# Performance work log

Hardware: AMD Instinct MI355X
Metric: run time of the kernel (lower is better)

## Reference

```python
import jax, jax.numpy as jnp
import numpy as np

# Spec constants (from init_kwargs)
NUM_ANCHORS = 5
NUM_CLASSES = 80
FM_H = 19
FM_W = 19
MAX_OBJECT = 50
NOOBJECT_SCALE = 1.0
OBJECT_SCALE = 5.0
BACKGROUND_THRESHOLD = 0.6
COORD_SCALE = 1.0
CLASS_SCALE = 1.0


def _iou_cwh(a, b):
    """IoU for boxes in (cx, cy, w, h) format; broadcasts over leading dims.
    Matches bbox_iou(..., x1y1x2y2=False) in the torch repo (0 when no overlap)."""
    ax1, ax2 = a[..., 0] - a[..., 2] * 0.5, a[..., 0] + a[..., 2] * 0.5
    ay1, ay2 = a[..., 1] - a[..., 3] * 0.5, a[..., 1] + a[..., 3] * 0.5
    bx1, bx2 = b[..., 0] - b[..., 2] * 0.5, b[..., 0] + b[..., 2] * 0.5
    by1, by2 = b[..., 1] - b[..., 3] * 0.5, b[..., 1] + b[..., 3] * 0.5
    uw = jnp.maximum(ax2, bx2) - jnp.minimum(ax1, bx1)
    uh = jnp.maximum(ay2, by2) - jnp.minimum(ay1, by1)
    cw = a[..., 2] + b[..., 2] - uw
    ch = a[..., 3] + b[..., 3] - uh
    inter = jnp.where((cw > 0) & (ch > 0), cw * ch, 0.0)
    union = a[..., 2] * a[..., 3] + b[..., 2] * b[..., 3] - inter
    return inter / jnp.maximum(union, 1e-12)


def setup_inputs() -> dict:
    key = jax.random.key(0)
    k1, k2, k3, k4, k5 = jax.random.split(key, 5)
    B, A, C, H, W, T = 64, NUM_ANCHORS, NUM_CLASSES, FM_H, FM_W, MAX_OBJECT
    output = jax.random.normal(k1, (B, A * (5 + C), H, W), jnp.float32) * 0.5
    # targets: per object (class, cx, cy, w, h), normalized to [0,1]; list ends at first cx == 0
    cls_t = jax.random.randint(k2, (B, T), 0, C).astype(jnp.float32)
    xy = jax.random.uniform(k3, (B, T, 2), jnp.float32, minval=0.1, maxval=0.9)
    wh = jax.random.uniform(k4, (B, T, 2), jnp.float32, minval=0.05, maxval=0.4)
    nvalid = jax.random.randint(k5, (B,), 1, T + 1)
    valid = (jnp.arange(T)[None, :] < nvalid[:, None]).astype(jnp.float32)
    tgt = jnp.concatenate([cls_t[..., None], xy, wh], axis=-1) * valid[..., None]
    target = tgt.reshape(B, T * 5)
    anchors = jnp.array([[1.3221, 1.73145], [3.19275, 4.00944], [5.05587, 8.09892],
                         [9.47112, 4.84053], [11.2364, 10.0071]], jnp.float32)
    return {"output": output, "target": target, "anchors": anchors}


def reference(output, target, anchors):
    B = output.shape[0]
    A, C, H, W, T = NUM_ANCHORS, NUM_CLASSES, FM_H, FM_W, MAX_OBJECT
    out = output.reshape(B, A, 5 + C, H, W)
    x = jax.nn.sigmoid(out[:, :, 0])
    y = jax.nn.sigmoid(out[:, :, 1])
    w = out[:, :, 2]
    h = out[:, :, 3]
    conf = jax.nn.sigmoid(out[:, :, 4])
    cls_logits = jnp.transpose(out[:, :, 5:], (0, 1, 3, 4, 2))  # [B,A,H,W,C]

    # decoded predicted boxes in grid units (detached for target building, as in torch)
    px = x + jnp.arange(W, dtype=x.dtype)[None, None, None, :]
    py = y + jnp.arange(H, dtype=x.dtype)[None, None, :, None]
    pw = jnp.exp(w) * anchors[None, :, 0, None, None]
    ph = jnp.exp(h) * anchors[None, :, 1, None, None]
    pred = jax.lax.stop_gradient(jnp.stack([px, py, pw, ph], axis=-1))  # [B,A,H,W,4]

    tgt = target.reshape(B, T, 5)
    cls_t = tgt[..., 0]
    gx = tgt[..., 1] * W
    gy = tgt[..., 2] * H
    gw = tgt[..., 3] * W
    gh = tgt[..., 4] * H
    # break-at-first-zero semantics of the torch loop
    valid = jnp.cumprod((tgt[..., 1] != 0).astype(jnp.int32), axis=1).astype(bool)  # [B,T]

    gt_boxes = jnp.stack([gx, gy, gw, gh], axis=-1)  # [B,T,4]
    # all-pairs pred-vs-gt IoU (replaces per-object python loop)
    pred_flat = pred.reshape(B, A * H * W, 4)
    ious = _iou_cwh(pred_flat[:, :, None, :], gt_boxes[:, None, :, :])  # [B,N,T]
    best_iou = jnp.max(jnp.where(valid[:, None, :], ious, 0.0), axis=-1)  # [B,N]
    conf_mask = jnp.where(best_iou > BACKGROUND_THRESHOLD, 0.0, NOOBJECT_SCALE)
    conf_mask = conf_mask.reshape(B, A, H, W)

    # best anchor per gt: IoU of (w,h) boxes centered at origin
    aw = anchors[:, 0][None, None, :]
    ah = anchors[:, 1][None, None, :]
    inter_a = jnp.minimum(gw[..., None], aw) * jnp.minimum(gh[..., None], ah)
    union_a = gw[..., None] * gh[..., None] + aw * ah - inter_a
    best_n = jnp.argmax(inter_a / jnp.maximum(union_a, 1e-12), axis=-1)  # [B,T]

    gi = jnp.clip(gx.astype(jnp.int32), 0, W - 1)
    gj = jnp.clip(gy.astype(jnp.int32), 0, H - 1)
    bidx = jnp.arange(B)[:, None]
    pred_sel = pred[bidx, best_n, gj, gi]  # [B,T,4]
    iou_obj = _iou_cwh(gt_boxes, pred_sel)  # [B,T]

    N = B * A * H * W
    flat = ((bidx * A + best_n) * H + gj) * W + gi  # [B,T]
    flat = jnp.where(valid, flat, N).reshape(-1)  # invalid -> out of range, dropped

    def scat(vals):
        return jnp.zeros((N,), jnp.float32).at[flat].set(
            vals.reshape(-1), mode="drop").reshape(B, A, H, W)

    coord_mask = scat(jnp.ones_like(gx))
    cls_mask = coord_mask
    conf_mask = conf_mask.reshape(-1).at[flat].set(
        jnp.full((B * T,), OBJECT_SCALE, jnp.float32), mode="drop").reshape(B, A, H, W)
    tx = scat(gx - gi.astype(gx.dtype))
    ty = scat(gy - gj.astype(gy.dtype))
    tw = scat(jnp.log(jnp.maximum(gw, 1e-12) / anchors[best_n, 0]))
    th = scat(jnp.log(jnp.maximum(gh, 1e-12) / anchors[best_n, 1]))
    tconf = scat(iou_obj)
    tcls = scat(cls_t)

    # losses (sum reduction, matching MSELoss/CrossEntropyLoss(size_average=False))
    loss_x = COORD_SCALE * jnp.sum((coord_mask * (x - tx)) ** 2) / 2.0
    loss_y = COORD_SCALE * jnp.sum((coord_mask * (y - ty)) ** 2) / 2.0
    loss_w = COORD_SCALE * jnp.sum((coord_mask * (w - tw)) ** 2) / 2.0
    loss_h = COORD_SCALE * jnp.sum((coord_mask * (h - th)) ** 2) / 2.0
    sq = jnp.sqrt(conf_mask)
    loss_conf = jnp.sum((sq * (conf - tconf)) ** 2) / 2.0
    ce = -jnp.take_along_axis(jax.nn.log_softmax(cls_logits, axis=-1),
                              tcls.astype(jnp.int32)[..., None], axis=-1)[..., 0]
    loss_cls = CLASS_SCALE * jnp.sum(cls_mask * ce)
    return loss_x + loss_y + loss_w + loss_h + loss_conf + loss_cls
```

## Files before the change

### kernel.cpp

```cpp
#include <hip/hip_runtime.h>
#include <math.h>

#define NUM_ANCHORS 5
#define NUM_CLASSES 80
#define FM_H 19
#define FM_W 19
#define MAX_OBJECT 50
#define HW (FM_H * FM_W)
#define CELLS_PER_B (NUM_ANCHORS * HW)
#define CH (5 + NUM_CLASSES)
#define THREADS 512
#define NW (THREADS / 64)
#define BLOCKS_PER_B ((CELLS_PER_B + THREADS - 1) / THREADS)
#define OBJECT_SCALE 5.0f
#define BACKGROUND_THRESHOLD 0.6f

__device__ inline float frcp(float v) { return __builtin_amdgcn_rcpf(v); }
__device__ inline float fsigmoid(float v) { return frcp(1.0f + __expf(-v)); }

__global__ __launch_bounds__(THREADS) void yolov2_main(
    const float* __restrict__ out,
    const float* __restrict__ target,
    const float* __restrict__ anchors,
    float* __restrict__ partial)
{
    const int b    = blockIdx.x / BLOCKS_PER_B;
    const int blk  = blockIdx.x % BLOCKS_PER_B;
    const int cell = blk * THREADS + threadIdx.x;
    const int lane = threadIdx.x & 63;
    const int wid  = threadIdx.x >> 6;

    __shared__ float4 gA[MAX_OBJECT];
    __shared__ float4 gB[MAX_OBJECT];
    __shared__ float4 gT[MAX_OBJECT];
    __shared__ int    entries[MAX_OBJECT];
    __shared__ int    nv_sh, ne_sh;
    __shared__ float  wsum[NW];

    const bool incell = (cell < CELLS_PER_B);
    const int a    = incell ? (cell / HW) : 0;
    const int hw   = cell - a * HW;
    const int hrow = hw / FM_W;
    const int wcol = hw - hrow * FM_W;

    const float* base = out + ((size_t)(b * NUM_ANCHORS + a) * CH) * HW + hw;
    float ox = 0.f, oy = 0.f, ow = 0.f, oh = 0.f, oc = 0.f;
    if (incell) {
        ox = base[0];
        oy = base[HW];
        ow = base[2 * HW];
        oh = base[3 * HW];
        oc = base[4 * HW];
    }
    const float anc_w = anchors[2 * a];
    const float anc_h = anchors[2 * a + 1];

    if (threadIdx.x < 64) {
        const int t = threadIdx.x;
        float f0 = 0.f, f1 = 0.f, f2 = 0.f, f3 = 0.f, f4 = 0.f;
        if (t < MAX_OBJECT) {
            const float* tp = target + (size_t)b * MAX_OBJECT * 5 + t * 5;
            f0 = tp[0]; f1 = tp[1]; f2 = tp[2]; f3 = tp[3]; f4 = tp[4];
        }
        unsigned long long m = __ballot(t < MAX_OBJECT && f1 != 0.0f);
        int nv = __popcll(m);
        if (t == 0) nv_sh = nv;

        int acell = 0x7FFFFFFF;
        int icls = 0;
        if (t < MAX_OBJECT) {
            float gx = f1 * (float)FM_W;
            float gy = f2 * (float)FM_H;
            float gw = f3 * (float)FM_W;
            float gh = f4 * (float)FM_H;
            int bn = 0; float best = -1.0f;
            #pragma unroll
            for (int k = 0; k < NUM_ANCHORS; ++k) {
                float aw = anchors[2 * k], ah = anchors[2 * k + 1];
                float inter = fminf(gw, aw) * fminf(gh, ah);
                float uni = gw * gh + aw * ah - inter;
                float r = inter * frcp(fmaxf(uni, 1e-12f));
                if (r > best) { best = r; bn = k; }
            }
            int gi = (int)gx; gi = gi < 0 ? 0 : (gi > FM_W - 1 ? FM_W - 1 : gi);
            int gj = (int)gy; gj = gj < 0 ? 0 : (gj > FM_H - 1 ? FM_H - 1 : gj);
            acell = bn * HW + gj * FM_W + gi;
            icls  = (int)f0;
            gA[t] = make_float4(gx - gw * 0.5f, gx + gw * 0.5f,
                                gy - gh * 0.5f, gy + gh * 0.5f);
            gB[t] = make_float4(gw, gh, gw * gh, __int_as_float(acell));
            gT[t] = make_float4(gx - (float)gi, gy - (float)gj,
                                __logf(fmaxf(gw, 1e-12f) * frcp(anchors[2 * bn])),
                                __logf(fmaxf(gh, 1e-12f) * frcp(anchors[2 * bn + 1])));
        }

        bool owner = (t < nv);
        #pragma unroll
        for (int s = 1; s < MAX_OBJECT; ++s) {
            int other = __shfl(acell, (t + s) & 63, 64);
            owner = owner && !((t + s < nv) && (other == acell));
        }
        bool keep = owner && ((acell >> 9) == blk);
        unsigned long long om = __ballot(keep);
        int pos = __popcll(om & ((1ull << t) - 1ull));
        if (keep) entries[pos] = acell | (icls << 16);
        if (t == 0) ne_sh = __popcll(om);
    }
    __syncthreads();

    const int nv = nv_sh;
    const int ne = ne_sh;
    float local = 0.0f;

    const bool ld = (lane < NUM_CLASSES / 2);
    int  eCur = wid;
    bool hasP = (eCur < ne);
    float pv0 = 0.f, pv1 = 0.f;
    int   pcls = 0;
    if (hasP) {
        int pk = entries[eCur];
        int ec = pk & 0xFFFF;
        pcls   = pk >> 16;
        int ea = ec / HW;
        const float* cl = out + ((size_t)(b * NUM_ANCHORS + ea) * CH + 5) * HW
                              + (ec - ea * HW);
        pv0 = ld ? cl[(2 * lane + 0) * HW] : 0.0f;
        pv1 = ld ? cl[(2 * lane + 1) * HW] : 0.0f;
    }

    if (incell) {
        float x    = fsigmoid(ox);
        float y    = fsigmoid(oy);
        float conf = fsigmoid(oc);
        float px = x + (float)wcol;
        float py = y + (float)hrow;
        float pw = __expf(ow) * anc_w;
        float ph = __expf(oh) * anc_h;
        float ax1 = px - pw * 0.5f, ax2 = px + pw * 0.5f;
        float ay1 = py - ph * 0.5f, ay2 = py + ph * 0.5f;
        float parea = pw * ph;

        bool bg_hit = false;
        int  last_t = -1;
        #pragma unroll 5
        for (int t = 0; t < nv; ++t) {
            float4 A  = gA[t];
            float4 Bv = gB[t];
            float uw = fmaxf(ax2, A.y) - fminf(ax1, A.x);
            float uh = fmaxf(ay2, A.w) - fminf(ay1, A.z);
            float cw  = Bv.x + pw - uw;
            float chh = Bv.y + ph - uh;
            float inter = (cw > 0.f && chh > 0.f) ? cw * chh : 0.f;
            float uni = parea + Bv.z - inter;
            bg_hit = bg_hit || (inter > BACKGROUND_THRESHOLD * uni);
            if (__float_as_int(Bv.w) == cell) last_t = t;
        }

        if (last_t >= 0) {
            float4 A  = gA[last_t];
            float4 Bv = gB[last_t];
            float4 Tt = gT[last_t];
            float uw = fmaxf(ax2, A.y) - fminf(ax1, A.x);
            float uh = fmaxf(ay2, A.w) - fminf(ay1, A.z);
            float cw  = Bv.x + pw - uw;
            float chh = Bv.y + ph - uh;
            float inter = (cw > 0.f && chh > 0.f) ? cw * chh : 0.f;
            float tconf = inter * frcp(fmaxf(parea + Bv.z - inter, 1e-12f));
            float dc = conf - tconf; local += 0.5f * OBJECT_SCALE * dc * dc;
            float dx = x  - Tt.x; local += 0.5f * dx * dx;
            float dy = y  - Tt.y; local += 0.5f * dy * dy;
            float dw = ow - Tt.z; local += 0.5f * dw * dw;
            float dh = oh - Tt.w; local += 0.5f * dh * dh;
        } else if (!bg_hit) {
            local += 0.5f * conf * conf;
        }
    }

    while (hasP) {
        int  eNxt = eCur + NW;
        bool hasN = (eNxt < ne);
        float nv0 = 0.f, nv1 = 0.f;
        int   ncls = 0;
        if (hasN) {
            int pk = entries[eNxt];
            int ec = pk & 0xFFFF;
            ncls   = pk >> 16;
            int ea = ec / HW;
            const float* cl = out + ((size_t)(b * NUM_ANCHORS + ea) * CH + 5) * HW
                                  + (ec - ea * HW);
            nv0 = ld ? cl[(2 * lane + 0) * HW] : 0.0f;
            nv1 = ld ? cl[(2 * lane + 1) * HW] : 0.0f;
        }
        float s = ld ? (__expf(pv0) + __expf(pv1)) : 0.0f;
        #pragma unroll
        for (int off = 32; off > 0; off >>= 1)
            s += __shfl_xor(s, off, 64);
        float tsel = (pcls & 1) ? pv1 : pv0;
        float tl = __shfl(tsel, pcls >> 1, 64);
        if (lane == 0) local += (__logf(s) - tl);

        pv0 = nv0; pv1 = nv1; pcls = ncls;
        eCur = eNxt; hasP = hasN;
    }

    #pragma unroll
    for (int off = 32; off > 0; off >>= 1)
        local += __shfl_down(local, off, 64);
    if (lane == 0) wsum[wid] = local;
    __syncthreads();
    if (threadIdx.x == 0) {
        float tot = 0.0f;
        #pragma unroll
        for (int i = 0; i < NW; ++i) tot += wsum[i];
        partial[blockIdx.x] = tot;
    }
}

__global__ __launch_bounds__(64) void yolov2_reduce(
    const float* __restrict__ partial, int n, float* __restrict__ loss)
{
    const float4* p4 = (const float4*)partial;
    float v = 0.0f;
    for (int i = threadIdx.x; i * 4 < n; i += 64) {
        float4 q = p4[i];
        v += (q.x + q.y) + (q.z + q.w);
    }
    #pragma unroll
    for (int off = 32; off > 0; off >>= 1)
        v += __shfl_down(v, off, 64);
    if (threadIdx.x == 0) loss[0] = v;
}

extern "C" void kernel_launch(void* const* d_in, const int* in_sizes, int n_in,
                              void* d_out, int out_size, void* d_ws, size_t ws_size,
                              hipStream_t stream) {
    const float* out_t   = (const float*)d_in[0];
    const float* target  = (const float*)d_in[1];
    const float* anchors = (const float*)d_in[2];
    float* loss    = (float*)d_out;
    float* partial = (float*)d_ws;

    const int B = in_sizes[1] / (MAX_OBJECT * 5);
    const int nblocks = B * BLOCKS_PER_B;

    yolov2_main<<<dim3(nblocks), dim3(THREADS), 0, stream>>>(out_t, target, anchors, partial);
    yolov2_reduce<<<dim3(1), dim3(64), 0, stream>>>(partial, nblocks, loss);
}
```

Before: 17.67 us.

## Fuse final reduction via atomics and replace owner shuffle scan with LDS map

```diff
diff --git a/kernel.cpp b/kernel.cpp
--- a/kernel.cpp
+++ b/kernel.cpp
@@ -13,16 +13,15 @@
 #define NW (THREADS / 64)
 #define BLOCKS_PER_B ((CELLS_PER_B + THREADS - 1) / THREADS)
 #define OBJECT_SCALE 5.0f
-#define BACKGROUND_THRESHOLD 0.6f
 
 __device__ inline float frcp(float v) { return __builtin_amdgcn_rcpf(v); }
 __device__ inline float fsigmoid(float v) { return frcp(1.0f + __expf(-v)); }
 
-__global__ __launch_bounds__(THREADS) void yolov2_main(
+__global__ __launch_bounds__(THREADS) void yolov2_fused(
     const float* __restrict__ out,
     const float* __restrict__ target,
     const float* __restrict__ anchors,
-    float* __restrict__ partial)
+    float* __restrict__ loss)
 {
     const int b    = blockIdx.x / BLOCKS_PER_B;
     const int blk  = blockIdx.x % BLOCKS_PER_B;
@@ -33,9 +32,13 @@
     __shared__ float4 gA[MAX_OBJECT];
     __shared__ float4 gB[MAX_OBJECT];
     __shared__ float4 gT[MAX_OBJECT];
+    __shared__ float  gZ[MAX_OBJECT];
+    __shared__ int    owner_map[CELLS_PER_B];
     __shared__ int    entries[MAX_OBJECT];
     __shared__ int    nv_sh, ne_sh;
     __shared__ float  wsum[NW];
+
+    if (blockIdx.x == 0 && threadIdx.x == 0) atomicExch(loss, 0.0f);
 
     const bool incell = (cell < CELLS_PER_B);
     const int a    = incell ? (cell / HW) : 0;
@@ -57,6 +60,9 @@
 
     if (threadIdx.x < 64) {
         const int t = threadIdx.x;
+        #pragma unroll
+        for (int i = t; i < CELLS_PER_B; i += 64) owner_map[i] = -1;
+
         float f0 = 0.f, f1 = 0.f, f2 = 0.f, f3 = 0.f, f4 = 0.f;
         if (t < MAX_OBJECT) {
             const float* tp = target + (size_t)b * MAX_OBJECT * 5 + t * 5;
@@ -66,8 +72,7 @@
         int nv = __popcll(m);
         if (t == 0) nv_sh = nv;
 
-        int acell = 0x7FFFFFFF;
-        int icls = 0;
+        int acell = 0, icls = 0;
         if (t < MAX_OBJECT) {
             float gx = f1 * (float)FM_W;
             float gy = f2 * (float)FM_H;
@@ -86,21 +91,19 @@
             int gj = (int)gy; gj = gj < 0 ? 0 : (gj > FM_H - 1 ? FM_H - 1 : gj);
             acell = bn * HW + gj * FM_W + gi;
             icls  = (int)f0;
+            float barea = gw * gh;
             gA[t] = make_float4(gx - gw * 0.5f, gx + gw * 0.5f,
                                 gy - gh * 0.5f, gy + gh * 0.5f);
-            gB[t] = make_float4(gw, gh, gw * gh, __int_as_float(acell));
+            gB[t] = make_float4(gw, gh, barea, 0.f);
+            gZ[t] = 0.6f * barea;
             gT[t] = make_float4(gx - (float)gi, gy - (float)gj,
                                 __logf(fmaxf(gw, 1e-12f) * frcp(anchors[2 * bn])),
                                 __logf(fmaxf(gh, 1e-12f) * frcp(anchors[2 * bn + 1])));
         }
-
-        bool owner = (t < nv);
-        #pragma unroll
-        for (int s = 1; s < MAX_OBJECT; ++s) {
-            int other = __shfl(acell, (t + s) & 63, 64);
-            owner = owner && !((t + s < nv) && (other == acell));
-        }
-        bool keep = owner && ((acell >> 9) == blk);
+        asm volatile("s_waitcnt lgkmcnt(0)" ::: "memory");
+        if (t < nv) atomicMax(&owner_map[acell], t);
+        asm volatile("s_waitcnt lgkmcnt(0)" ::: "memory");
+        bool keep = (t < nv) && (owner_map[acell] == t) && ((acell >> 9) == blk);
         unsigned long long om = __ballot(keep);
         int pos = __popcll(om & ((1ull << t) - 1ull));
         if (keep) entries[pos] = acell | (icls << 16);
@@ -112,7 +115,7 @@
     const int ne = ne_sh;
     float local = 0.0f;
 
-    const bool ld = (lane < NUM_CLASSES / 2);
+    const bool ld2 = (lane < NUM_CLASSES / 2);
     int  eCur = wid;
     bool hasP = (eCur < ne);
     float pv0 = 0.f, pv1 = 0.f;
@@ -124,8 +127,8 @@
         int ea = ec / HW;
         const float* cl = out + ((size_t)(b * NUM_ANCHORS + ea) * CH + 5) * HW
                               + (ec - ea * HW);
-        pv0 = ld ? cl[(2 * lane + 0) * HW] : 0.0f;
-        pv1 = ld ? cl[(2 * lane + 1) * HW] : 0.0f;
+        pv0 = ld2 ? cl[(2 * lane + 0) * HW] : 0.0f;
+        pv1 = ld2 ? cl[(2 * lane + 1) * HW] : 0.0f;
     }
 
     if (incell) {
@@ -139,32 +142,27 @@
         float ax1 = px - pw * 0.5f, ax2 = px + pw * 0.5f;
         float ay1 = py - ph * 0.5f, ay2 = py + ph * 0.5f;
         float parea = pw * ph;
+        float p6 = 0.6f * parea;
 
         bool bg_hit = false;
-        int  last_t = -1;
         #pragma unroll 5
         for (int t = 0; t < nv; ++t) {
-            float4 A  = gA[t];
-            float4 Bv = gB[t];
-            float uw = fmaxf(ax2, A.y) - fminf(ax1, A.x);
-            float uh = fmaxf(ay2, A.w) - fminf(ay1, A.z);
-            float cw  = Bv.x + pw - uw;
-            float chh = Bv.y + ph - uh;
-            float inter = (cw > 0.f && chh > 0.f) ? cw * chh : 0.f;
-            float uni = parea + Bv.z - inter;
-            bg_hit = bg_hit || (inter > BACKGROUND_THRESHOLD * uni);
-            if (__float_as_int(Bv.w) == cell) last_t = t;
-        }
-
-        if (last_t >= 0) {
-            float4 A  = gA[last_t];
-            float4 Bv = gB[last_t];
-            float4 Tt = gT[last_t];
-            float uw = fmaxf(ax2, A.y) - fminf(ax1, A.x);
-            float uh = fmaxf(ay2, A.w) - fminf(ay1, A.z);
-            float cw  = Bv.x + pw - uw;
-            float chh = Bv.y + ph - uh;
-            float inter = (cw > 0.f && chh > 0.f) ? cw * chh : 0.f;
+            float4 A = gA[t];
+            float cwx = fminf(ax2, A.y) - fmaxf(ax1, A.x);
+            float cwy = fminf(ay2, A.w) - fmaxf(ay1, A.z);
+            float inter = cwx * cwy;
+            bg_hit = bg_hit ||
+                     ((cwx > 0.f) && (cwy > 0.f) && (1.6f * inter > p6 + gZ[t]));
+        }
+
+        const int own = owner_map[cell];
+        if (own >= 0) {
+            float4 A  = gA[own];
+            float4 Bv = gB[own];
+            float4 Tt = gT[own];
+            float cwx = fminf(ax2, A.y) - fmaxf(ax1, A.x);
+            float cwy = fminf(ay2, A.w) - fmaxf(ay1, A.z);
+            float inter = (cwx > 0.f && cwy > 0.f) ? cwx * cwy : 0.f;
             float tconf = inter * frcp(fmaxf(parea + Bv.z - inter, 1e-12f));
             float dc = conf - tconf; local += 0.5f * OBJECT_SCALE * dc * dc;
             float dx = x  - Tt.x; local += 0.5f * dx * dx;
@@ -188,10 +186,10 @@
             int ea = ec / HW;
             const float* cl = out + ((size_t)(b * NUM_ANCHORS + ea) * CH + 5) * HW
                                   + (ec - ea * HW);
-            nv0 = ld ? cl[(2 * lane + 0) * HW] : 0.0f;
-            nv1 = ld ? cl[(2 * lane + 1) * HW] : 0.0f;
-        }
-        float s = ld ? (__expf(pv0) + __expf(pv1)) : 0.0f;
+            nv0 = ld2 ? cl[(2 * lane + 0) * HW] : 0.0f;
+            nv1 = ld2 ? cl[(2 * lane + 1) * HW] : 0.0f;
+        }
+        float s = ld2 ? (__expf(pv0) + __expf(pv1)) : 0.0f;
         #pragma unroll
         for (int off = 32; off > 0; off >>= 1)
             s += __shfl_xor(s, off, 64);
@@ -212,23 +210,8 @@
         float tot = 0.0f;
         #pragma unroll
         for (int i = 0; i < NW; ++i) tot += wsum[i];
-        partial[blockIdx.x] = tot;
-    }
-}
-
-__global__ __launch_bounds__(64) void yolov2_reduce(
-    const float* __restrict__ partial, int n, float* __restrict__ loss)
-{
-    const float4* p4 = (const float4*)partial;
-    float v = 0.0f;
-    for (int i = threadIdx.x; i * 4 < n; i += 64) {
-        float4 q = p4[i];
-        v += (q.x + q.y) + (q.z + q.w);
-    }
-    #pragma unroll
-    for (int off = 32; off > 0; off >>= 1)
-        v += __shfl_down(v, off, 64);
-    if (threadIdx.x == 0) loss[0] = v;
+        atomicAdd(loss, tot);
+    }
 }
 
 extern "C" void kernel_launch(void* const* d_in, const int* in_sizes, int n_in,
@@ -237,12 +220,11 @@
     const float* out_t   = (const float*)d_in[0];
     const float* target  = (const float*)d_in[1];
     const float* anchors = (const float*)d_in[2];
-    float* loss    = (float*)d_out;
-    float* partial = (float*)d_ws;
+    float* loss          = (float*)d_out;
 
     const int B = in_sizes[1] / (MAX_OBJECT * 5);
     const int nblocks = B * BLOCKS_PER_B;
 
-    yolov2_main<<<dim3(nblocks), dim3(THREADS), 0, stream>>>(out_t, target, anchors, partial);
-    yolov2_reduce<<<dim3(1), dim3(64), 0, stream>>>(partial, nblocks, loss);
+    yolov2_fused<<<dim3(nblocks), dim3(THREADS), 0, stream>>>(
+        out_t, target, anchors, loss);
 }
```

Result: no change. 17.68 us (+0.1%).
